# Performance work log

Measured on AMD Instinct MI355X. Metric: run time of the kernel, lower is better.

Reference implementation:

```python
import jax, jax.numpy as jnp
import numpy as np

B, M, N, D, H = 4, 8, 128, 32, 64
SMALL_V = 1e-8


def setup_inputs() -> dict:
    key = jax.random.key(0)
    ks = jax.random.split(key, 12)
    s = 0.05
    x = jax.random.normal(ks[0], (B, M, N, D), jnp.float32)
    sizes = jax.random.randint(ks[1], (B,), N // 2, N + 1)
    valid = (jnp.arange(N)[None, :] < sizes[:, None]).astype(jnp.float32)  # [B,N]
    x = x * valid[:, None, :, None]  # zero out padded items
    return {
        "x": x,
        "x_size": sizes.astype(jnp.float32),
        "W1a": jax.random.normal(ks[2], (D, 2 * D), jnp.float32) * s,
        "b1a": jax.random.normal(ks[3], (2 * D,), jnp.float32) * s,
        "W1b": jax.random.normal(ks[4], (2 * D, D), jnp.float32) * s,
        "b1b": jax.random.normal(ks[5], (D,), jnp.float32) * s,
        "W2a": jax.random.normal(ks[6], (D, 2 * D), jnp.float32) * s,
        "b2a": jax.random.normal(ks[7], (2 * D,), jnp.float32) * s,
        "W2b": jax.random.normal(ks[8], (2 * D, H), jnp.float32) * s,
        "b2b": jax.random.normal(ks[9], (H,), jnp.float32) * s,
        "w3": jax.random.normal(ks[10], (H,), jnp.float32) * s,
        "b3": jax.random.normal(ks[11], (1,), jnp.float32) * s,
    }


def _item_mask(x):
    # 1.0 where the item's feature row has any nonzero entry, else 0.0. [...,N,1]
    return jnp.any(x != 0, axis=-1, keepdims=True).astype(x.dtype)


def _set_norm(x, x_size):
    # layer_normalization with is_set_norm=True: normalize over (N*D) per set,
    # dividing by the true valid size x_size*D and masking padded items.
    b, m, n, d = x.shape
    mask = jnp.broadcast_to(_item_mask(x), x.shape).reshape(b, m, n * d)
    xr = x.reshape(b, m, n * d)
    denom = x_size[:, None] * d  # [B,1] -> broadcasts over nSet
    mean = jnp.sum(xr, axis=-1) / denom  # [B,M]
    diff = xr - mean[..., None]
    std = jnp.sqrt(jnp.sum(diff * diff * mask, axis=-1) / denom)  # [B,M]
    out = diff / (std[..., None] + SMALL_V) * mask
    return out.reshape(b, m, n, d)


def reference(x, x_size, W1a, b1a, W1b, b1b, W2a, b2a, W2b, b2b, w3, b3):
    mask = _item_mask(x)  # [B,M,N,1]
    x_orig = x
    xn = _set_norm(x, x_size) * mask  # [B,M,N,D]
    # MLP1 (rank-4 -> masked by its own input's item mask)
    m1 = _item_mask(xn)
    x1 = (jnp.matmul(jax.nn.gelu(jnp.matmul(xn, W1a) + b1a), W1b) + b1b) * m1
    # pairwise differences: x_diff[b,m,i,j,:] = x1[b,m,i,:] - xn[b,m,j,:]
    x_diff = x1[:, :, :, None, :] - xn[:, :, None, :, :]  # [B,M,N,N,D]
    # MLP2 (rank-5 -> no mask, is_SoftMax=0)
    e = jnp.matmul(jax.nn.gelu(jnp.matmul(x_diff, W2a) + b2a), W2b) + b2b  # [B,M,N,N,H]
    # aggregation: out[b,m,j,h,d] = sum_i e[b,m,i,j,h] * x1[b,m,i,d]
    agg = jnp.einsum('bmijh,bmid->bmjhd', e, x1)
    # MLP3_linear: Dense(1) over H, then squeeze
    out = jnp.einsum('bmjhd,h->bmjd', agg, w3) + b3[0]
    out = (out + x_orig) * mask
    return out
```

## Files before the change

### kernel.cpp

```cpp
#include <hip/hip_runtime.h>

#define BB 4
#define MM 8
#define BM 32
#define NN 128
#define DD 32
#define KK 64
constexpr int ND = NN * DD;
constexpr int NK = NN * KK;
#define SMALLV 1e-8f

__device__ __forceinline__ float gelu_t(float v) {
    float v2 = v * v;
    float u  = v * fmaf(0.044715f, v2, 1.0f) * 0.7978845608028654f;
    float e  = __builtin_amdgcn_exp2f(u * 2.8853900817779268f);
    float r  = __builtin_amdgcn_rcpf(e + 1.0f);
    float th = fmaf(-2.0f, r, 1.0f);
    float hv = 0.5f * v;
    return fmaf(hv, th, hv);
}

__global__ __launch_bounds__(512) void stats_kernel(
    const float* __restrict__ x, const float* __restrict__ x_size,
    float* __restrict__ statsg, float* __restrict__ maskg)
{
    __shared__ float sAny[NN];
    __shared__ float sRed[8];
    const int t = threadIdx.x, bm = blockIdx.x;
    const float* xp = x + (size_t)bm * ND;
    float v[8];
    float lsum = 0.f;
    #pragma unroll
    for (int s = 0; s < 8; ++s) { v[s] = xp[t + s * 512]; lsum += v[s]; }
    if (t < NN) sAny[t] = 0.f;
    __syncthreads();
    #pragma unroll
    for (int s = 0; s < 8; ++s) if (v[s] != 0.f) sAny[(t + s * 512) >> 5] = 1.f;
    #pragma unroll
    for (int off = 32; off; off >>= 1) lsum += __shfl_xor(lsum, off);
    if ((t & 63) == 0) sRed[t >> 6] = lsum;
    __syncthreads();
    float tot = 0.f;
    #pragma unroll
    for (int w = 0; w < 8; ++w) tot += sRed[w];
    const float denom = x_size[bm >> 3] * (float)DD;
    const float mean  = tot / denom;
    float lsq = 0.f;
    #pragma unroll
    for (int s = 0; s < 8; ++s) {
        float d = v[s] - mean;
        lsq += (sAny[(t + s * 512) >> 5] != 0.f) ? d * d : 0.f;
    }
    #pragma unroll
    for (int off = 32; off; off >>= 1) lsq += __shfl_xor(lsq, off);
    __syncthreads();
    if ((t & 63) == 0) sRed[t >> 6] = lsq;
    __syncthreads();
    float sq = 0.f;
    #pragma unroll
    for (int w = 0; w < 8; ++w) sq += sRed[w];
    const float inv = 1.f / (sqrtf(sq / denom) + SMALLV);
    if (t == 0) { statsg[bm * 2] = mean; statsg[bm * 2 + 1] = inv; }
    if (t < NN) maskg[bm * NN + t] = sAny[t];
}

__global__ __launch_bounds__(256) void mlp_kernel(
    const float* __restrict__ x, const float* __restrict__ statsg,
    const float* __restrict__ maskg,
    const float* __restrict__ W1a, const float* __restrict__ b1a,
    const float* __restrict__ W1b, const float* __restrict__ b1b,
    const float* __restrict__ W2a, const float* __restrict__ b2a,
    const float* __restrict__ W2b, const float* __restrict__ b2b,
    const float* __restrict__ w3,
    float* __restrict__ x1g, float* __restrict__ A1g, float* __restrict__ A2t,
    float* __restrict__ v2g, float* __restrict__ c3g)
{
    __shared__ float sW1a[DD * KK];
    __shared__ float sW1b[KK * DD];
    __shared__ float sW2a[DD * KK];
    __shared__ float sXn[8 * DD];
    __shared__ float sH[8 * KK];
    __shared__ float sX1[8 * DD];
    __shared__ float sB1a[KK], sB2a[KK], sB1b[DD];

    const int t  = threadIdx.x;
    const int bm = blockIdx.x >> 4;
    const int nt = blockIdx.x & 15;
    const int n0 = nt * 8;
    const float mean = statsg[bm * 2], inv = statsg[bm * 2 + 1];

    {
        const float4* a4 = (const float4*)W1a;
        const float4* b4 = (const float4*)W1b;
        const float4* c4 = (const float4*)W2a;
        float4* sa = (float4*)sW1a; float4* sb = (float4*)sW1b; float4* sc = (float4*)sW2a;
        sa[t] = a4[t]; sa[t + 256] = a4[t + 256];
        sb[t] = b4[t]; sb[t + 256] = b4[t + 256];
        sc[t] = c4[t]; sc[t + 256] = c4[t + 256];
    }
    if (t < KK) { sB1a[t] = b1a[t]; sB2a[t] = b2a[t]; }
    if (t < DD) { sB1b[t] = b1b[t]; }

    {
        float mk = maskg[bm * NN + n0 + (t >> 5)];
        float xv = x[(size_t)bm * ND + n0 * DD + t];
        sXn[t] = (xv - mean) * inv * mk;
    }
    __syncthreads();

    const int k    = t & 63;
    const int slot = t >> 6;

    #pragma unroll
    for (int r = 0; r < 2; ++r) {
        int n = slot + r * 4;
        const float* xr = &sXn[n * DD];
        float acc = sB1a[k];
        #pragma unroll
        for (int d = 0; d < DD; ++d) acc = fmaf(xr[d], sW1a[d * KK + k], acc);
        sH[n * KK + k] = gelu_t(acc);
    }
    __syncthreads();

    {
        const int d2 = t & 31;
        const int n  = t >> 5;
        const float* hr = &sH[n * KK];
        float acc = sB1b[d2];
        #pragma unroll
        for (int q = 0; q < KK; ++q) acc = fmaf(hr[q], sW1b[q * DD + d2], acc);
        float val = acc * maskg[bm * NN + n0 + n];
        sX1[n * DD + d2] = val;
        x1g[(size_t)bm * ND + (n0 + n) * DD + d2] = val;
    }
    __syncthreads();

    #pragma unroll
    for (int r = 0; r < 2; ++r) {
        int n = slot + r * 4;
        const float* x1r = &sX1[n * DD];
        const float* xnr = &sXn[n * DD];
        float a1 = sB2a[k], a2 = 0.f;
        #pragma unroll
        for (int d = 0; d < DD; ++d) {
            a1 = fmaf(x1r[d], sW2a[d * KK + k], a1);
            a2 = fmaf(xnr[d], sW2a[d * KK + k], a2);
        }
        A1g[(size_t)bm * NK + (n0 + n) * KK + k] = a1;
        A2t[(size_t)bm * NK + k * NN + (n0 + n)] = a2;
    }

    if (blockIdx.x == 0) {
        if (t < KK) {
            float acc = 0.f;
            for (int h = 0; h < KK; ++h) acc += W2b[t * KK + h] * w3[h];
            v2g[t] = acc;
        }
        if (t == 0) {
            float acc = 0.f;
            for (int h = 0; h < KK; ++h) acc += b2b[h] * w3[h];
            c3g[0] = acc;
        }
    }
}

__global__ __launch_bounds__(256) void pair_kernel(
    const float* __restrict__ A1g, const float* __restrict__ A2t,
    const float* __restrict__ x1g, const float* __restrict__ v2g,
    const float* __restrict__ c3g, float* __restrict__ partial)
{
    __shared__ float sA1[8 * KK];
    __shared__ float sX1[8 * DD];
    __shared__ float sV2[KK];
    __shared__ float sPart[4][64][DD + 1];
    const int t    = threadIdx.x;
    const int bm   = blockIdx.x >> 5;
    const int jg   = (blockIdx.x >> 4) & 1;
    const int ig   = blockIdx.x & 15;
    const int w    = t >> 6;
    const int lane = t & 63;

    sA1[t]       = A1g[(size_t)bm * NK + ig * 512 + t];
    sA1[t + 256] = A1g[(size_t)bm * NK + ig * 512 + t + 256];
    sX1[t]       = x1g[(size_t)bm * ND + ig * 256 + t];
    if (t < KK) sV2[t] = v2g[t];
    const float c3 = c3g[0];

    float a2r[KK];
    #pragma unroll
    for (int q = 0; q < KK; ++q)
        a2r[q] = A2t[(size_t)bm * NK + q * NN + jg * 64 + lane];

    float acc[DD];
    #pragma unroll
    for (int d = 0; d < DD; ++d) acc[d] = 0.f;
    __syncthreads();

    const float4* v2f = (const float4*)sV2;
    {
        const int i0 = w * 2, i1 = w * 2 + 1;
        const float4* a1f0 = (const float4*)&sA1[i0 * KK];
        const float4* a1f1 = (const float4*)&sA1[i1 * KK];
        const float4* x1f0 = (const float4*)&sX1[i0 * DD];
        const float4* x1f1 = (const float4*)&sX1[i1 * DD];
        float S0 = c3, S1 = c3;
        #pragma unroll
        for (int kq = 0; kq < 16; ++kq) {
            float4 a0 = a1f0[kq];
            float4 a1 = a1f1[kq];
            float4 vv = v2f[kq];
            S0 = fmaf(gelu_t(a0.x - a2r[kq * 4 + 0]), vv.x, S0);
            S1 = fmaf(gelu_t(a1.x - a2r[kq * 4 + 0]), vv.x, S1);
            S0 = fmaf(gelu_t(a0.y - a2r[kq * 4 + 1]), vv.y, S0);
            S1 = fmaf(gelu_t(a1.y - a2r[kq * 4 + 1]), vv.y, S1);
            S0 = fmaf(gelu_t(a0.z - a2r[kq * 4 + 2]), vv.z, S0);
            S1 = fmaf(gelu_t(a1.z - a2r[kq * 4 + 2]), vv.z, S1);
            S0 = fmaf(gelu_t(a0.w - a2r[kq * 4 + 3]), vv.w, S0);
            S1 = fmaf(gelu_t(a1.w - a2r[kq * 4 + 3]), vv.w, S1);
        }
        #pragma unroll
        for (int dq = 0; dq < 8; ++dq) {
            float4 xa = x1f0[dq];
            float4 xb = x1f1[dq];
            acc[dq * 4 + 0] = fmaf(S0, xa.x, fmaf(S1, xb.x, acc[dq * 4 + 0]));
            acc[dq * 4 + 1] = fmaf(S0, xa.y, fmaf(S1, xb.y, acc[dq * 4 + 1]));
            acc[dq * 4 + 2] = fmaf(S0, xa.z, fmaf(S1, xb.z, acc[dq * 4 + 2]));
            acc[dq * 4 + 3] = fmaf(S0, xa.w, fmaf(S1, xb.w, acc[dq * 4 + 3]));
        }
    }
    #pragma unroll
    for (int d = 0; d < DD; ++d) sPart[w][lane][d] = acc[d];
    __syncthreads();

    const size_t base = (size_t)blockIdx.x * 2048;
    #pragma unroll
    for (int s = 0; s < 8; ++s) {
        int idx = t + s * 256;
        int jl = idx >> 5, d = idx & 31;
        partial[base + idx] =
            sPart[0][jl][d] + sPart[1][jl][d] + sPart[2][jl][d] + sPart[3][jl][d];
    }
}

__global__ __launch_bounds__(256) void final_kernel(
    const float* __restrict__ x, const float* __restrict__ b3,
    const float* __restrict__ partial, float* __restrict__ out)
{
    const int gid = blockIdx.x * 256 + threadIdx.x;
    const int j = gid >> 5;
    const int bm = j >> 7, jg = (j >> 6) & 1, jl = j & 63;
    const size_t pb = ((size_t)(bm * 2 + jg) * 16) * 2048 + (jl << 5) + (gid & 31);
    float sum = 0.f;
    #pragma unroll
    for (int ig = 0; ig < 16; ++ig) sum += partial[pb + ig * 2048];
    float xv = x[gid];
    unsigned long long bal = __ballot(xv != 0.f);
    int lane = threadIdx.x & 63;
    unsigned long long half = (lane < 32) ? (bal & 0xFFFFFFFFull) : (bal >> 32);
    float mk = half ? 1.f : 0.f;
    out[gid] = (sum + b3[0] + xv) * mk;
}

extern "C" void kernel_launch(void* const* d_in, const int* in_sizes, int n_in,
                              void* d_out, int out_size, void* d_ws, size_t ws_size,
                              hipStream_t stream) {
    const float* x      = (const float*)d_in[0];
    const float* x_size = (const float*)d_in[1];
    const float* W1a    = (const float*)d_in[2];
    const float* b1a    = (const float*)d_in[3];
    const float* W1b    = (const float*)d_in[4];
    const float* b1b    = (const float*)d_in[5];
    const float* W2a    = (const float*)d_in[6];
    const float* b2a    = (const float*)d_in[7];
    const float* W2b    = (const float*)d_in[8];
    const float* b2b    = (const float*)d_in[9];
    const float* w3     = (const float*)d_in[10];
    const float* b3     = (const float*)d_in[11];
    float* out = (float*)d_out;

    float* ws      = (float*)d_ws;
    float* statsg  = ws;
    float* maskg   = statsg + 64;
    float* x1g     = maskg + 4096;
    float* A1g     = x1g + (size_t)BM * ND;
    float* A2t     = A1g + (size_t)BM * NK;
    float* v2g     = A2t + (size_t)BM * NK;
    float* c3g     = v2g + KK;
    float* partial = c3g + 64;

    stats_kernel<<<BM, 512, 0, stream>>>(x, x_size, statsg, maskg);
    mlp_kernel<<<BM * 16, 256, 0, stream>>>(x, statsg, maskg,
        W1a, b1a, W1b, b1b, W2a, b2a, W2b, b2b, w3,
        x1g, A1g, A2t, v2g, c3g);
    pair_kernel<<<BM * 32, 256, 0, stream>>>(A1g, A2t, x1g, v2g, c3g, partial);
    final_kernel<<<512, 256, 0, stream>>>(x, b3, partial, out);
}
```

Before: 108.1 us.

## Fuse set-norm stats into MLP kernel and restructure pair kernel work split

Removes the separate stats kernel: each MLP block recomputes the per-set mean, variance and item mask from the full set, which adds redundant reads of x across 16 blocks but saves a launch. The pair kernel now handles all 128 j per block with 4 i rows per wave, stages the S scores in shared memory and does a second pass for the D-aggregation, halving the block count and the partial-buffer layout. GELU is rewritten into a cheaper algebraically equivalent form using a folded polynomial and x*sigmoid.

```diff
diff --git a/kernel.cpp b/kernel.cpp
--- a/kernel.cpp
+++ b/kernel.cpp
@@ -1,72 +1,23 @@
 #include <hip/hip_runtime.h>
 
-#define BB 4
-#define MM 8
-#define BM 32
-#define NN 128
-#define DD 32
-#define KK 64
-constexpr int ND = NN * DD;
-constexpr int NK = NN * KK;
+#define BMC 32
+#define NNC 128
+#define DDC 32
+#define KKC 64
+constexpr int ND = NNC * DDC;
+constexpr int NK = NNC * KKC;
 #define SMALLV 1e-8f
 
-__device__ __forceinline__ float gelu_t(float v) {
+__device__ __forceinline__ float gelu_f(float v) {
     float v2 = v * v;
-    float u  = v * fmaf(0.044715f, v2, 1.0f) * 0.7978845608028654f;
-    float e  = __builtin_amdgcn_exp2f(u * 2.8853900817779268f);
+    float p  = fmaf(0.1029432f, v2, 2.3022082f);
+    float e  = __builtin_amdgcn_exp2f(v * p);
     float r  = __builtin_amdgcn_rcpf(e + 1.0f);
-    float th = fmaf(-2.0f, r, 1.0f);
-    float hv = 0.5f * v;
-    return fmaf(hv, th, hv);
-}
-
-__global__ __launch_bounds__(512) void stats_kernel(
+    return fmaf(-v, r, v);
+}
+
+__global__ __launch_bounds__(256) void mlp_kernel(
     const float* __restrict__ x, const float* __restrict__ x_size,
-    float* __restrict__ statsg, float* __restrict__ maskg)
-{
-    __shared__ float sAny[NN];
-    __shared__ float sRed[8];
-    const int t = threadIdx.x, bm = blockIdx.x;
-    const float* xp = x + (size_t)bm * ND;
-    float v[8];
-    float lsum = 0.f;
-    #pragma unroll
-    for (int s = 0; s < 8; ++s) { v[s] = xp[t + s * 512]; lsum += v[s]; }
-    if (t < NN) sAny[t] = 0.f;
-    __syncthreads();
-    #pragma unroll
-    for (int s = 0; s < 8; ++s) if (v[s] != 0.f) sAny[(t + s * 512) >> 5] = 1.f;
-    #pragma unroll
-    for (int off = 32; off; off >>= 1) lsum += __shfl_xor(lsum, off);
-    if ((t & 63) == 0) sRed[t >> 6] = lsum;
-    __syncthreads();
-    float tot = 0.f;
-    #pragma unroll
-    for (int w = 0; w < 8; ++w) tot += sRed[w];
-    const float denom = x_size[bm >> 3] * (float)DD;
-    const float mean  = tot / denom;
-    float lsq = 0.f;
-    #pragma unroll
-    for (int s = 0; s < 8; ++s) {
-        float d = v[s] - mean;
-        lsq += (sAny[(t + s * 512) >> 5] != 0.f) ? d * d : 0.f;
-    }
-    #pragma unroll
-    for (int off = 32; off; off >>= 1) lsq += __shfl_xor(lsq, off);
-    __syncthreads();
-    if ((t & 63) == 0) sRed[t >> 6] = lsq;
-    __syncthreads();
-    float sq = 0.f;
-    #pragma unroll
-    for (int w = 0; w < 8; ++w) sq += sRed[w];
-    const float inv = 1.f / (sqrtf(sq / denom) + SMALLV);
-    if (t == 0) { statsg[bm * 2] = mean; statsg[bm * 2 + 1] = inv; }
-    if (t < NN) maskg[bm * NN + t] = sAny[t];
-}
-
-__global__ __launch_bounds__(256) void mlp_kernel(
-    const float* __restrict__ x, const float* __restrict__ statsg,
-    const float* __restrict__ maskg,
     const float* __restrict__ W1a, const float* __restrict__ b1a,
     const float* __restrict__ W1b, const float* __restrict__ b1b,
     const float* __restrict__ W2a, const float* __restrict__ b2a,
@@ -75,19 +26,21 @@
     float* __restrict__ x1g, float* __restrict__ A1g, float* __restrict__ A2t,
     float* __restrict__ v2g, float* __restrict__ c3g)
 {
-    __shared__ float sW1a[DD * KK];
-    __shared__ float sW1b[KK * DD];
-    __shared__ float sW2a[DD * KK];
-    __shared__ float sXn[8 * DD];
-    __shared__ float sH[8 * KK];
-    __shared__ float sX1[8 * DD];
-    __shared__ float sB1a[KK], sB2a[KK], sB1b[DD];
+    __shared__ float sW1a[DDC * KKC];
+    __shared__ float sW1b[KKC * DDC];
+    __shared__ float sW2a[DDC * KKC];
+    __shared__ float sXn[8 * DDC];
+    __shared__ float sH[8 * KKC];
+    __shared__ float sX1[8 * DDC];
+    __shared__ float sB1a[KKC], sB2a[KKC], sB1b[DDC];
+    __shared__ float sAny[NNC];
+    __shared__ float sRed[4];
 
     const int t  = threadIdx.x;
     const int bm = blockIdx.x >> 4;
     const int nt = blockIdx.x & 15;
     const int n0 = nt * 8;
-    const float mean = statsg[bm * 2], inv = statsg[bm * 2 + 1];
+    const int w  = t >> 6;
 
     {
         const float4* a4 = (const float4*)W1a;
@@ -98,67 +51,103 @@
         sb[t] = b4[t]; sb[t + 256] = b4[t + 256];
         sc[t] = c4[t]; sc[t + 256] = c4[t + 256];
     }
-    if (t < KK) { sB1a[t] = b1a[t]; sB2a[t] = b2a[t]; }
-    if (t < DD) { sB1b[t] = b1b[t]; }
+    if (t < KKC) { sB1a[t] = b1a[t]; sB2a[t] = b2a[t]; }
+    if (t < DDC) { sB1b[t] = b1b[t]; }
+    if (t < NNC) sAny[t] = 0.f;
+    __syncthreads();
+
+    const float4* xs4 = (const float4*)(x + (size_t)bm * ND);
+    float4 v4[4];
+    float lsum = 0.f;
+    #pragma unroll
+    for (int s = 0; s < 4; ++s) {
+        int f = t + s * 256;
+        float4 q = xs4[f];
+        v4[s] = q;
+        lsum += q.x + q.y + q.z + q.w;
+        if (q.x != 0.f || q.y != 0.f || q.z != 0.f || q.w != 0.f) sAny[f >> 3] = 1.f;
+    }
+    #pragma unroll
+    for (int off = 32; off; off >>= 1) lsum += __shfl_xor(lsum, off);
+    if ((t & 63) == 0) sRed[w] = lsum;
+    __syncthreads();
+    const float denom = x_size[bm >> 3] * (float)DDC;
+    const float mean  = (sRed[0] + sRed[1] + sRed[2] + sRed[3]) / denom;
+
+    float lsq = 0.f;
+    #pragma unroll
+    for (int s = 0; s < 4; ++s) {
+        int f = t + s * 256;
+        float mk = sAny[f >> 3];
+        float dx = v4[s].x - mean, dy = v4[s].y - mean;
+        float dz = v4[s].z - mean, dw = v4[s].w - mean;
+        lsq += mk * (dx * dx + dy * dy + dz * dz + dw * dw);
+    }
+    #pragma unroll
+    for (int off = 32; off; off >>= 1) lsq += __shfl_xor(lsq, off);
+    __syncthreads();
+    if ((t & 63) == 0) sRed[w] = lsq;
+    __syncthreads();
+    const float sq  = sRed[0] + sRed[1] + sRed[2] + sRed[3];
+    const float inv = 1.f / (sqrtf(sq / denom) + SMALLV);
 
     {
-        float mk = maskg[bm * NN + n0 + (t >> 5)];
-        float xv = x[(size_t)bm * ND + n0 * DD + t];
-        sXn[t] = (xv - mean) * inv * mk;
+        float xv = x[(size_t)bm * ND + n0 * DDC + t];
+        sXn[t] = (xv - mean) * inv * sAny[n0 + (t >> 5)];
     }
     __syncthreads();
 
     const int k    = t & 63;
-    const int slot = t >> 6;
+    const int slot = w;
 
     #pragma unroll
     for (int r = 0; r < 2; ++r) {
         int n = slot + r * 4;
-        const float* xr = &sXn[n * DD];
+        const float* xr = &sXn[n * DDC];
         float acc = sB1a[k];
         #pragma unroll
-        for (int d = 0; d < DD; ++d) acc = fmaf(xr[d], sW1a[d * KK + k], acc);
-        sH[n * KK + k] = gelu_t(acc);
+        for (int d = 0; d < DDC; ++d) acc = fmaf(xr[d], sW1a[d * KKC + k], acc);
+        sH[n * KKC + k] = gelu_f(acc);
     }
     __syncthreads();
 
     {
         const int d2 = t & 31;
         const int n  = t >> 5;
-        const float* hr = &sH[n * KK];
+        const float* hr = &sH[n * KKC];
         float acc = sB1b[d2];
         #pragma unroll
-        for (int q = 0; q < KK; ++q) acc = fmaf(hr[q], sW1b[q * DD + d2], acc);
-        float val = acc * maskg[bm * NN + n0 + n];
-        sX1[n * DD + d2] = val;
-        x1g[(size_t)bm * ND + (n0 + n) * DD + d2] = val;
+        for (int q = 0; q < KKC; ++q) acc = fmaf(hr[q], sW1b[q * DDC + d2], acc);
+        float val = acc * sAny[n0 + n];
+        sX1[n * DDC + d2] = val;
+        x1g[(size_t)bm * ND + (n0 + n) * DDC + d2] = val;
     }
     __syncthreads();
 
     #pragma unroll
     for (int r = 0; r < 2; ++r) {
         int n = slot + r * 4;
-        const float* x1r = &sX1[n * DD];
-        const float* xnr = &sXn[n * DD];
+        const float* x1r = &sX1[n * DDC];
+        const float* xnr = &sXn[n * DDC];
         float a1 = sB2a[k], a2 = 0.f;
         #pragma unroll
-        for (int d = 0; d < DD; ++d) {
-            a1 = fmaf(x1r[d], sW2a[d * KK + k], a1);
-            a2 = fmaf(xnr[d], sW2a[d * KK + k], a2);
-        }
-        A1g[(size_t)bm * NK + (n0 + n) * KK + k] = a1;
-        A2t[(size_t)bm * NK + k * NN + (n0 + n)] = a2;
+        for (int d = 0; d < DDC; ++d) {
+            a1 = fmaf(x1r[d], sW2a[d * KKC + k], a1);
+            a2 = fmaf(xnr[d], sW2a[d * KKC + k], a2);
+        }
+        A1g[(size_t)bm * NK + (n0 + n) * KKC + k] = a1;
+        A2t[(size_t)bm * NK + k * NNC + (n0 + n)] = a2;
     }
 
     if (blockIdx.x == 0) {
-        if (t < KK) {
+        if (t < KKC) {
             float acc = 0.f;
-            for (int h = 0; h < KK; ++h) acc += W2b[t * KK + h] * w3[h];
+            for (int h = 0; h < KKC; ++h) acc += W2b[t * KKC + h] * w3[h];
             v2g[t] = acc;
         }
         if (t == 0) {
             float acc = 0.f;
-            for (int h = 0; h < KK; ++h) acc += b2b[h] * w3[h];
+            for (int h = 0; h < KKC; ++h) acc += b2b[h] * w3[h];
             c3g[0] = acc;
         }
     }
@@ -169,77 +158,68 @@
     const float* __restrict__ x1g, const float* __restrict__ v2g,
     const float* __restrict__ c3g, float* __restrict__ partial)
 {
-    __shared__ float sA1[8 * KK];
-    __shared__ float sX1[8 * DD];
-    __shared__ float sV2[KK];
-    __shared__ float sPart[4][64][DD + 1];
+    __shared__ float sS[8 * NNC];
+    __shared__ float sX1[8 * DDC];
     const int t    = threadIdx.x;
-    const int bm   = blockIdx.x >> 5;
-    const int jg   = (blockIdx.x >> 4) & 1;
+    const int bm   = blockIdx.x >> 4;
     const int ig   = blockIdx.x & 15;
-    const int w    = t >> 6;
+    const int w    = __builtin_amdgcn_readfirstlane(t >> 6);
     const int lane = t & 63;
-
-    sA1[t]       = A1g[(size_t)bm * NK + ig * 512 + t];
-    sA1[t + 256] = A1g[(size_t)bm * NK + ig * 512 + t + 256];
-    sX1[t]       = x1g[(size_t)bm * ND + ig * 256 + t];
-    if (t < KK) sV2[t] = v2g[t];
+    const int jg   = w & 1;
+    const int ih   = w >> 1;
+    const int ib   = ig * 8 + ih * 4;
+
+    sX1[t] = x1g[(size_t)bm * ND + ig * 8 * DDC + t];
+
+    const float* A2p = A2t + (size_t)bm * NK + jg * 64 + lane;
+    float a2r[KKC];
+    #pragma unroll
+    for (int q = 0; q < KKC; ++q) a2r[q] = A2p[q * NNC];
+
+    const float* a1p0 = A1g + (size_t)bm * NK + (ib + 0) * KKC;
+    const float* a1p1 = A1g + (size_t)bm * NK + (ib + 1) * KKC;
+    const float* a1p2 = A1g + (size_t)bm * NK + (ib + 2) * KKC;
+    const float* a1p3 = A1g + (size_t)bm * NK + (ib + 3) * KKC;
     const float c3 = c3g[0];
 
-    float a2r[KK];
-    #pragma unroll
-    for (int q = 0; q < KK; ++q)
-        a2r[q] = A2t[(size_t)bm * NK + q * NN + jg * 64 + lane];
-
-    float acc[DD];
-    #pragma unroll
-    for (int d = 0; d < DD; ++d) acc[d] = 0.f;
-    __syncthreads();
-
-    const float4* v2f = (const float4*)sV2;
-    {
-        const int i0 = w * 2, i1 = w * 2 + 1;
-        const float4* a1f0 = (const float4*)&sA1[i0 * KK];
-        const float4* a1f1 = (const float4*)&sA1[i1 * KK];
-        const float4* x1f0 = (const float4*)&sX1[i0 * DD];
-        const float4* x1f1 = (const float4*)&sX1[i1 * DD];
-        float S0 = c3, S1 = c3;
-        #pragma unroll
-        for (int kq = 0; kq < 16; ++kq) {
-            float4 a0 = a1f0[kq];
-            float4 a1 = a1f1[kq];
-            float4 vv = v2f[kq];
-            S0 = fmaf(gelu_t(a0.x - a2r[kq * 4 + 0]), vv.x, S0);
-            S1 = fmaf(gelu_t(a1.x - a2r[kq * 4 + 0]), vv.x, S1);
-            S0 = fmaf(gelu_t(a0.y - a2r[kq * 4 + 1]), vv.y, S0);
-            S1 = fmaf(gelu_t(a1.y - a2r[kq * 4 + 1]), vv.y, S1);
-            S0 = fmaf(gelu_t(a0.z - a2r[kq * 4 + 2]), vv.z, S0);
-            S1 = fmaf(gelu_t(a1.z - a2r[kq * 4 + 2]), vv.z, S1);
-            S0 = fmaf(gelu_t(a0.w - a2r[kq * 4 + 3]), vv.w, S0);
-            S1 = fmaf(gelu_t(a1.w - a2r[kq * 4 + 3]), vv.w, S1);
-        }
-        #pragma unroll
-        for (int dq = 0; dq < 8; ++dq) {
-            float4 xa = x1f0[dq];
-            float4 xb = x1f1[dq];
-            acc[dq * 4 + 0] = fmaf(S0, xa.x, fmaf(S1, xb.x, acc[dq * 4 + 0]));
-            acc[dq * 4 + 1] = fmaf(S0, xa.y, fmaf(S1, xb.y, acc[dq * 4 + 1]));
-            acc[dq * 4 + 2] = fmaf(S0, xa.z, fmaf(S1, xb.z, acc[dq * 4 + 2]));
-            acc[dq * 4 + 3] = fmaf(S0, xa.w, fmaf(S1, xb.w, acc[dq * 4 + 3]));
-        }
-    }
-    #pragma unroll
-    for (int d = 0; d < DD; ++d) sPart[w][lane][d] = acc[d];
-    __syncthreads();
-
-    const size_t base = (size_t)blockIdx.x * 2048;
-    #pragma unroll
-    for (int s = 0; s < 8; ++s) {
-        int idx = t + s * 256;
-        int jl = idx >> 5, d = idx & 31;
-        partial[base + idx] =
-            sPart[0][jl][d] + sPart[1][jl][d] + sPart[2][jl][d] + sPart[3][jl][d];
-    }
+    float S0 = c3, S1 = c3, S2 = c3, S3 = c3;
+    #pragma unroll
+    for (int kk = 0; kk < KKC; ++kk) {
+        const float vk = v2g[kk];
+        S0 = fmaf(gelu_f(a1p0[kk] - a2r[kk]), vk, S0);
+        S1 = fmaf(gelu_f(a1p1[kk] - a2r[kk]), vk, S1);
+        S2 = fmaf(gelu_f(a1p2[kk] - a2r[kk]), vk, S2);
+        S3 = fmaf(gelu_f(a1p3[kk] - a2r[kk]), vk, S3);
+    }
+    const int jcol = jg * 64 + lane;
+    sS[(ih * 4 + 0) * NNC + jcol] = S0;
+    sS[(ih * 4 + 1) * NNC + jcol] = S1;
+    sS[(ih * 4 + 2) * NNC + jcol] = S2;
+    sS[(ih * 4 + 3) * NNC + jcol] = S3;
+    __syncthreads();
+
+    const int j  = t >> 1;
+    const int dh = t & 1;
+    float acc[16];
+    #pragma unroll
+    for (int d = 0; d < 16; ++d) acc[d] = 0.f;
+    #pragma unroll
+    for (int i = 0; i < 8; ++i) {
+        float S = sS[i * NNC + j];
+        const float4* xf = (const float4*)&sX1[i * DDC + dh * 16];
+        #pragma unroll
+        for (int q = 0; q < 4; ++q) {
+            float4 xv = xf[q];
+            acc[q * 4 + 0] = fmaf(S, xv.x, acc[q * 4 + 0]);
+            acc[q * 4 + 1] = fmaf(S, xv.y, acc[q * 4 + 1]);
+            acc[q * 4 + 2] = fmaf(S, xv.z, acc[q * 4 + 2]);
+            acc[q * 4 + 3] = fmaf(S, xv.w, acc[q * 4 + 3]);
+        }
+    }
+    float4* pout = (float4*)(partial + ((size_t)(bm * 16 + ig) * NNC) * DDC + (size_t)t * 16);
+    #pragma unroll
+    for (int q = 0; q < 4; ++q)
+        pout[q] = make_float4(acc[q * 4 + 0], acc[q * 4 + 1], acc[q * 4 + 2], acc[q * 4 + 3]);
 }
 
 __global__ __launch_bounds__(256) void final_kernel(
@@ -247,12 +227,12 @@
     const float* __restrict__ partial, float* __restrict__ out)
 {
     const int gid = blockIdx.x * 256 + threadIdx.x;
-    const int j = gid >> 5;
-    const int bm = j >> 7, jg = (j >> 6) & 1, jl = j & 63;
-    const size_t pb = ((size_t)(bm * 2 + jg) * 16) * 2048 + (jl << 5) + (gid & 31);
+    const int bm  = gid >> 12;
+    const int rem = gid & 4095;
+    const size_t pb = (size_t)bm * 16 * 4096 + rem;
     float sum = 0.f;
     #pragma unroll
-    for (int ig = 0; ig < 16; ++ig) sum += partial[pb + ig * 2048];
+    for (int ig = 0; ig < 16; ++ig) sum += partial[pb + (size_t)ig * 4096];
     float xv = x[gid];
     unsigned long long bal = __ballot(xv != 0.f);
     int lane = threadIdx.x & 63;
@@ -279,19 +259,16 @@
     float* out = (float*)d_out;
 
     float* ws      = (float*)d_ws;
-    float* statsg  = ws;
-    float* maskg   = statsg + 64;
-    float* x1g     = maskg + 4096;
-    float* A1g     = x1g + (size_t)BM * ND;
-    float* A2t     = A1g + (size_t)BM * NK;
-    float* v2g     = A2t + (size_t)BM * NK;
-    float* c3g     = v2g + KK;
+    float* x1g     = ws;
+    float* A1g     = x1g + (size_t)BMC * ND;
+    float* A2t     = A1g + (size_t)BMC * NK;
+    float* v2g     = A2t + (size_t)BMC * NK;
+    float* c3g     = v2g + KKC;
     float* partial = c3g + 64;
 
-    stats_kernel<<<BM, 512, 0, stream>>>(x, x_size, statsg, maskg);
-    mlp_kernel<<<BM * 16, 256, 0, stream>>>(x, statsg, maskg,
+    mlp_kernel<<<BMC * 16, 256, 0, stream>>>(x, x_size,
         W1a, b1a, W1b, b1b, W2a, b2a, W2b, b2b, w3,
         x1g, A1g, A2t, v2g, c3g);
-    pair_kernel<<<BM * 32, 256, 0, stream>>>(A1g, A2t, x1g, v2g, c3g, partial);
+    pair_kernel<<<BMC * 16, 256, 0, stream>>>(A1g, A2t, x1g, v2g, c3g, partial);
     final_kernel<<<512, 256, 0, stream>>>(x, b3, partial, out);
 }
```

Result: faster. 104.7 us (-3.2%).
